# Performance work log

Hardware: AMD Instinct MI355X
Metric: run time of the kernel (lower is better)

Reference implementation:

```python
import jax, jax.numpy as jnp
import numpy as np

T, B, D, H, NQ = 512, 128, 512, 64, 64  # seq_len, batch, input_dim, hidden_dim == n_qubits
EPS = 1e-5

def setup_inputs() -> dict:
    key = jax.random.key(0)
    ks = jax.random.split(key, 11)
    s = 0.05
    return {
        "inputs": jax.random.normal(ks[0], (T, B, D), jnp.float32),
        "W0": jax.random.normal(ks[1], (4, NQ, D + H), jnp.float32) * s,
        "b0": jax.random.normal(ks[2], (4, NQ), jnp.float32) * s,
        "th0": jax.random.normal(ks[3], (4, NQ), jnp.float32) * s,
        "g0": jnp.ones((H,), jnp.float32),
        "be0": jnp.zeros((H,), jnp.float32),
        "W1": jax.random.normal(ks[4], (4, NQ, H + H), jnp.float32) * s,
        "b1": jax.random.normal(ks[5], (4, NQ), jnp.float32) * s,
        "th1": jax.random.normal(ks[6], (4, NQ), jnp.float32) * s,
        "g1": jnp.ones((H,), jnp.float32),
        "be1": jnp.zeros((H,), jnp.float32),
    }

def _qlstm_layer(x, W, b, th, gamma, beta):
    # x: [T, B, Din]. Faithful to source: h_prev = c_prev = 0 at EVERY timestep
    # (the torch code never writes back `states` inside the time loop), so all
    # timesteps are independent and fully vectorized.
    zeros_h = jnp.zeros(x.shape[:-1] + (H,), x.dtype)
    combined = jnp.concatenate([x, zeros_h], axis=-1)           # [T,B,Din+H]
    # 4 gate linears stacked on leading axis g: forget, input, update, output
    z = jnp.einsum('tbk,gnk->gtbn', combined, W) + b[:, None, None, :]
    # quantum circuit closed form: RX(z_i+th_i) per qubit + CNOT ladder + <Z_k>
    #   => cumprod_{i<=k} cos(z_i + th_i)
    q = jnp.cumprod(jnp.cos(z + th[:, None, None, :]), axis=-1)  # [4,T,B,NQ]
    sg = jax.nn.sigmoid(q)
    i_g = sg[1]
    g_g = jnp.tanh(sg[2])
    o_g = sg[3]
    # c = f * c_prev + i * g, with c_prev == 0  (f gate has no effect)
    c = i_g * g_g                                                # [T,B,H]
    h = o_g * jnp.tanh(c)
    mu = jnp.mean(h, axis=-1, keepdims=True)
    var = jnp.mean((h - mu) ** 2, axis=-1, keepdims=True)
    h_ln = (h - mu) * jax.lax.rsqrt(var + EPS) * gamma + beta
    return h_ln, c

def reference(inputs, W0, b0, th0, g0, be0, W1, b1, th1, g1, be1):
    h0, c0 = _qlstm_layer(inputs, W0, b0, th0, g0, be0)  # layer 0 (no dropout: p=0)
    h1, c1 = _qlstm_layer(h0, W1, b1, th1, g1, be1)      # layer 1
    outputs = h1                                          # [T,B,H]
    # new_states = states at the last timestep: [(h_ln, c)] per layer
    return (outputs, h0[-1], c0[-1], h1[-1], c1[-1])
```

## Files before the change

kernel.cpp:

```cpp
#include <hip/hip_runtime.h>
#include <hip/hip_bf16.h>

typedef __attribute__((ext_vector_type(8))) short bf16x8;
typedef __attribute__((ext_vector_type(4))) float f32x4;

#define T_SEQ   512
#define B_BATCH 128
#define H_DIM   64
#define MB      64
#define AS_STRIDE 136
#define ZS_STRIDE 193
#define A2S       72
#define LASTROW ((T_SEQ - 1) * B_BATCH)

#define W0H 0
#define W0M 98304
#define W0L 196608
#define W1H 294912
#define W1M 307200
#define W1L 319488

__device__ __forceinline__ void tsplit(float f, unsigned& h, unsigned& m, unsigned& l) {
    unsigned uf = __builtin_bit_cast(unsigned, f);
    h = uf >> 16;
    float hf = __builtin_bit_cast(float, uf & 0xFFFF0000u);
    float r1 = f - hf;
    unsigned u1 = __builtin_bit_cast(unsigned, r1);
    m = u1 >> 16;
    float mf = __builtin_bit_cast(float, u1 & 0xFFFF0000u);
    float r2 = r1 - mf;
    l = __builtin_bit_cast(unsigned, r2) >> 16;
}

__device__ __forceinline__ void tsplit2(float a, float b,
                                        unsigned& ph, unsigned& pm, unsigned& pl) {
    unsigned ha, ma, la, hb, mb, lb;
    tsplit(a, ha, ma, la);
    tsplit(b, hb, mb, lb);
    ph = ha | (hb << 16);
    pm = ma | (mb << 16);
    pl = la | (lb << 16);
}

__device__ __forceinline__ f32x4 mfma6(bf16x8 ah, bf16x8 am, bf16x8 al,
                                       bf16x8 bh, bf16x8 bm, bf16x8 bl, f32x4 c) {
    c = __builtin_amdgcn_mfma_f32_16x16x32_bf16(ah, bh, c, 0, 0, 0);
    c = __builtin_amdgcn_mfma_f32_16x16x32_bf16(ah, bm, c, 0, 0, 0);
    c = __builtin_amdgcn_mfma_f32_16x16x32_bf16(am, bh, c, 0, 0, 0);
    c = __builtin_amdgcn_mfma_f32_16x16x32_bf16(ah, bl, c, 0, 0, 0);
    c = __builtin_amdgcn_mfma_f32_16x16x32_bf16(al, bh, c, 0, 0, 0);
    c = __builtin_amdgcn_mfma_f32_16x16x32_bf16(am, bm, c, 0, 0, 0);
    return c;
}

__device__ __forceinline__ float fast_cos(float x) {
    float n = rintf(x * 0.6366197723675814f);
    int   m = (int)n;
    float r = __builtin_fmaf(n, -1.5707962512969971e+00f, x);
    r = __builtin_fmaf(n, -7.5497894158615964e-08f, r);
    r = __builtin_fmaf(n, -5.3903025299577647e-15f, r);
    float r2 = r * r;
    float ps = __builtin_fmaf(r2, 2.7557314297e-06f, -1.9841270114e-04f);
    ps = __builtin_fmaf(r2, ps, 8.3333337680e-03f);
    ps = __builtin_fmaf(r2, ps, -1.6666667163e-01f);
    float s = __builtin_fmaf(r * r2, ps, r);
    float pc = __builtin_fmaf(r2, 2.4801587642e-05f, -1.3888889225e-03f);
    pc = __builtin_fmaf(r2, pc, 4.1666667908e-02f);
    pc = __builtin_fmaf(r2, pc, -0.5f);
    float c = __builtin_fmaf(r2, pc, 1.0f);
    float v = (m & 1) ? s : c;
    unsigned sign = (unsigned)((m + 1) & 2) << 30;
    return __builtin_bit_cast(float, __builtin_bit_cast(unsigned, v) ^ sign);
}

__device__ __forceinline__ float fast_sigmoid(float x) {
    float e = __expf(-x);
    float d = 1.0f + e;
    float r = __builtin_amdgcn_rcpf(d);
    return r * (2.0f - d * r);
}

__device__ __forceinline__ float fast_tanh_pos(float x) {
    float t = __expf(2.0f * x);
    float d = t + 1.0f;
    float r = __builtin_amdgcn_rcpf(d);
    r = r * (2.0f - d * r);
    return (t - 1.0f) * r;
}

__global__ __launch_bounds__(256) void presplit_w(const float* __restrict__ W0,
                                                  const float* __restrict__ W1,
                                                  short* __restrict__ ws) {
    int i = blockIdx.x * 256 + threadIdx.x;
    if (i < 98304) {
        int r = i >> 9, k = i & 511;
        unsigned h, m, l;
        tsplit(W0[(r + 64) * 576 + k], h, m, l);
        ws[W0H + i] = (short)h;
        ws[W0M + i] = (short)m;
        ws[W0L + i] = (short)l;
    } else if (i < 110592) {
        int j = i - 98304;
        int r = j >> 6, k = j & 63;
        unsigned h, m, l;
        tsplit(W1[(r + 64) * 128 + k], h, m, l);
        ws[W1H + j] = (short)h;
        ws[W1M + j] = (short)m;
        ws[W1L + j] = (short)l;
    }
}

__global__ __launch_bounds__(256, 3) void qlstm_fused(
    const float* __restrict__ x,
    const float* __restrict__ b0,
    const float* __restrict__ th0,
    const float* __restrict__ g0,
    const float* __restrict__ be0,
    const float* __restrict__ b1,
    const float* __restrict__ th1,
    const float* __restrict__ g1,
    const float* __restrict__ be1,
    const short* __restrict__ wsp,
    float* __restrict__ out)
{
    __shared__ __align__(16) char lds[53760];
    short* ah = (short*)lds;
    short* am = ah + 64 * AS_STRIDE;
    short* al = am + 64 * AS_STRIDE;
    float* zs  = (float*)lds;
    short* a2h = (short*)lds;
    short* a2m = a2h + 64 * A2S;
    short* a2l = a2m + 64 * A2S;
    float* bt0 = (float*)(lds + 52224);
    float* bt1 = bt0 + 192;

    const int tid = threadIdx.x;
    const long rowbase = (long)blockIdx.x * MB;

    float* out0 = out;
    float* out1 = out + (long)T_SEQ * B_BATCH * H_DIM;
    float* out2 = out1 + B_BATCH * H_DIM;
    float* out3 = out2 + B_BATCH * H_DIM;
    float* out4 = out3 + B_BATCH * H_DIM;

    if (tid < 192) {
        bt0[tid] = b0[64 + tid] + th0[64 + tid];
        bt1[tid] = b1[64 + tid] + th1[64 + tid];
    }

    const int lane = tid & 63;
    const int wave = tid >> 6;
    const int ln   = lane & 15;
    const int quad = lane >> 4;
    const int cw   = wave * 48;

    int brow0[3], brow1[3];
    for (int nt = 0; nt < 3; ++nt) {
        int gc = cw + nt * 16 + ln;
        brow0[nt] = gc * 512;
        brow1[nt] = gc * 64;
    }

    f32x4 acc[4][3];
    for (int mt = 0; mt < 4; ++mt)
        for (int nt = 0; nt < 3; ++nt)
            acc[mt][nt] = (f32x4){0.f, 0.f, 0.f, 0.f};

    for (int kc = 0; kc < 512; kc += 128) {
        for (int pass = 0; pass < 4; ++pass) {
            int e  = pass * 256 + tid;
            int r  = e >> 4;
            int k8 = (e & 15) << 3;
            const float* xp = x + (rowbase + r) * 512 + kc + k8;
            float4 f0 = *(const float4*)xp;
            float4 f1 = *(const float4*)(xp + 4);
            uint4 Ph, Pm, Pl;
            tsplit2(f0.x, f0.y, Ph.x, Pm.x, Pl.x);
            tsplit2(f0.z, f0.w, Ph.y, Pm.y, Pl.y);
            tsplit2(f1.x, f1.y, Ph.z, Pm.z, Pl.z);
            tsplit2(f1.z, f1.w, Ph.w, Pm.w, Pl.w);
            int ao = r * AS_STRIDE + k8;
            *(uint4*)(ah + ao) = Ph;
            *(uint4*)(am + ao) = Pm;
            *(uint4*)(al + ao) = Pl;
        }
        __syncthreads();
        for (int k0 = 0; k0 < 128; k0 += 32) {
            int ka = k0 + quad * 8;
            bf16x8 Ah[4], Am[4], Al[4];
            for (int mt = 0; mt < 4; ++mt) {
                int ao = (mt * 16 + ln) * AS_STRIDE + ka;
                Ah[mt] = *(const bf16x8*)(ah + ao);
                Am[mt] = *(const bf16x8*)(am + ao);
                Al[mt] = *(const bf16x8*)(al + ao);
            }
            for (int nt = 0; nt < 3; ++nt) {
                int bo = brow0[nt] + kc + ka;
                bf16x8 Bh = *(const bf16x8*)(wsp + W0H + bo);
                bf16x8 Bm = *(const bf16x8*)(wsp + W0M + bo);
                bf16x8 Bl = *(const bf16x8*)(wsp + W0L + bo);
                for (int mt = 0; mt < 4; ++mt)
                    acc[mt][nt] = mfma6(Ah[mt], Am[mt], Al[mt], Bh, Bm, Bl, acc[mt][nt]);
            }
        }
        __syncthreads();
    }

    for (int mt = 0; mt < 4; ++mt)
        for (int nt = 0; nt < 3; ++nt)
            for (int i = 0; i < 4; ++i) {
                int row = mt * 16 + quad * 4 + i;
                int col = cw + nt * 16 + ln;
                zs[row * ZS_STRIDE + col] = acc[mt][nt][i];
            }
    __syncthreads();

    if (tid < 192) {
        int gi = tid >> 6;
        int r  = tid & 63;
        float* zrow = zs + r * ZS_STRIDE + gi * 64;
        const float* btg = bt0 + gi * 64;
        float p = 1.0f;
        for (int n = 0; n < 64; ++n) {
            p *= fast_cos(zrow[n] + btg[n]);
            zrow[n] = p;
        }
    }
    __syncthreads();

    {
        int r = tid >> 2;
        int j = tid & 3;
        long tbrow = rowbase + r;
        bool lastt = (tbrow >= LASTROW);
        int bidx = (int)(tbrow - LASTROW);
        const float* zr = zs + r * ZS_STRIDE;
        float h[16];
        float s = 0.f;
        for (int i = 0; i < 16; ++i) {
            int n = j * 16 + i;
            float q1 = zr[n];
            float q2 = zr[64 + n];
            float q3 = zr[128 + n];
            float ig = fast_sigmoid(q1);
            float gg = fast_tanh_pos(fast_sigmoid(q2));
            float og = fast_sigmoid(q3);
            float c  = ig * gg;
            float hv = og * fast_tanh_pos(c);
            h[i] = hv;
            s += hv;
            if (lastt) out2[bidx * 64 + n] = c;
        }
        s += __shfl_xor(s, 1);  s += __shfl_xor(s, 2);
        float mu = s * (1.0f / 64.0f);
        float s2 = 0.f;
        for (int i = 0; i < 16; ++i) {
            float d = h[i] - mu;
            s2 += d * d;
        }
        s2 += __shfl_xor(s2, 1); s2 += __shfl_xor(s2, 2);
        float var = s2 * (1.0f / 64.0f);
        float rs  = rsqrtf(var + 1e-5f);
        float hl[16];
        for (int i = 0; i < 16; ++i) {
            int n = j * 16 + i;
            hl[i] = (h[i] - mu) * rs * g0[n] + be0[n];
            if (lastt) out1[bidx * 64 + n] = hl[i];
        }
        __syncthreads();

        int ab = r * A2S + j * 16;
        uint4 Ph, Pm, Pl;
        tsplit2(hl[0], hl[1], Ph.x, Pm.x, Pl.x);
        tsplit2(hl[2], hl[3], Ph.y, Pm.y, Pl.y);
        tsplit2(hl[4], hl[5], Ph.z, Pm.z, Pl.z);
        tsplit2(hl[6], hl[7], Ph.w, Pm.w, Pl.w);
        *(uint4*)(a2h + ab) = Ph;
        *(uint4*)(a2m + ab) = Pm;
        *(uint4*)(a2l + ab) = Pl;
        tsplit2(hl[8],  hl[9],  Ph.x, Pm.x, Pl.x);
        tsplit2(hl[10], hl[11], Ph.y, Pm.y, Pl.y);
        tsplit2(hl[12], hl[13], Ph.z, Pm.z, Pl.z);
        tsplit2(hl[14], hl[15], Ph.w, Pm.w, Pl.w);
        *(uint4*)(a2h + ab + 8) = Ph;
        *(uint4*)(a2m + ab + 8) = Pm;
        *(uint4*)(a2l + ab + 8) = Pl;
    }
    __syncthreads();

    f32x4 acc2[4][3];
    for (int mt = 0; mt < 4; ++mt)
        for (int nt = 0; nt < 3; ++nt)
            acc2[mt][nt] = (f32x4){0.f, 0.f, 0.f, 0.f};
    for (int k0 = 0; k0 < 64; k0 += 32) {
        int ka = k0 + quad * 8;
        bf16x8 Ah[4], Am[4], Al[4];
        for (int mt = 0; mt < 4; ++mt) {
            int ao = (mt * 16 + ln) * A2S + ka;
            Ah[mt] = *(const bf16x8*)(a2h + ao);
            Am[mt] = *(const bf16x8*)(a2m + ao);
            Al[mt] = *(const bf16x8*)(a2l + ao);
        }
        for (int nt = 0; nt < 3; ++nt) {
            int bo = brow1[nt] + ka;
            bf16x8 Bh = *(const bf16x8*)(wsp + W1H + bo);
            bf16x8 Bm = *(const bf16x8*)(wsp + W1M + bo);
            bf16x8 Bl = *(const bf16x8*)(wsp + W1L + bo);
            for (int mt = 0; mt < 4; ++mt)
                acc2[mt][nt] = mfma6(Ah[mt], Am[mt], Al[mt], Bh, Bm, Bl, acc2[mt][nt]);
        }
    }
    __syncthreads();
    for (int mt = 0; mt < 4; ++mt)
        for (int nt = 0; nt < 3; ++nt)
            for (int i = 0; i < 4; ++i) {
                int row = mt * 16 + quad * 4 + i;
                int col = cw + nt * 16 + ln;
                zs[row * ZS_STRIDE + col] = acc2[mt][nt][i];
            }
    __syncthreads();

    if (tid < 192) {
        int gi = tid >> 6;
        int r  = tid & 63;
        float* zrow = zs + r * ZS_STRIDE + gi * 64;
        const float* btg = bt1 + gi * 64;
        float p = 1.0f;
        for (int n = 0; n < 64; ++n) {
            p *= fast_cos(zrow[n] + btg[n]);
            zrow[n] = p;
        }
    }
    __syncthreads();

    {
        int r = tid >> 2;
        int j = tid & 3;
        long tbrow = rowbase + r;
        bool lastt = (tbrow >= LASTROW);
        int bidx = (int)(tbrow - LASTROW);
        const float* zr = zs + r * ZS_STRIDE;
        float h[16];
        float s = 0.f;
        for (int i = 0; i < 16; ++i) {
            int n = j * 16 + i;
            float q1 = zr[n];
            float q2 = zr[64 + n];
            float q3 = zr[128 + n];
            float ig = fast_sigmoid(q1);
            float gg = fast_tanh_pos(fast_sigmoid(q2));
            float og = fast_sigmoid(q3);
            float c  = ig * gg;
            float hv = og * fast_tanh_pos(c);
            h[i] = hv;
            s += hv;
            if (lastt) out4[bidx * 64 + n] = c;
        }
        s += __shfl_xor(s, 1);  s += __shfl_xor(s, 2);
        float mu = s * (1.0f / 64.0f);
        float s2 = 0.f;
        for (int i = 0; i < 16; ++i) {
            float d = h[i] - mu;
            s2 += d * d;
        }
        s2 += __shfl_xor(s2, 1); s2 += __shfl_xor(s2, 2);
        float var = s2 * (1.0f / 64.0f);
        float rs  = rsqrtf(var + 1e-5f);
        float o4[16];
        for (int i = 0; i < 16; ++i)
            o4[i] = (h[i] - mu) * rs * g1[j * 16 + i] + be1[j * 16 + i];
        float* dst = out0 + tbrow * 64 + j * 16;
        for (int i4 = 0; i4 < 4; ++i4)
            *(float4*)(dst + i4 * 4) = *(float4*)(o4 + i4 * 4);
        if (lastt) {
            float* dst3 = out3 + (long)bidx * 64 + j * 16;
            for (int i4 = 0; i4 < 4; ++i4)
                *(float4*)(dst3 + i4 * 4) = *(float4*)(o4 + i4 * 4);
        }
    }
}

extern "C" void kernel_launch(void* const* d_in, const int* in_sizes, int n_in,
                              void* d_out, int out_size, void* d_ws, size_t ws_size,
                              hipStream_t stream) {
    const float* x   = (const float*)d_in[0];
    const float* W0  = (const float*)d_in[1];
    const float* b0  = (const float*)d_in[2];
    const float* th0 = (const float*)d_in[3];
    const float* g0  = (const float*)d_in[4];
    const float* be0 = (const float*)d_in[5];
    const float* W1  = (const float*)d_in[6];
    const float* b1  = (const float*)d_in[7];
    const float* th1 = (const float*)d_in[8];
    const float* g1  = (const float*)d_in[9];
    const float* be1 = (const float*)d_in[10];
    short* wsp = (short*)d_ws;

    presplit_w<<<dim3(432), dim3(256), 0, stream>>>(W0, W1, wsp);
    qlstm_fused<<<dim3(1024), dim3(256), 0, stream>>>(
        x, b0, th0, g0, be0, b1, th1, g1, be1, wsp, (float*)d_out);
}
```

Baseline: 323.2 us.

## Prefetch next input K-chunk into registers during MFMA on current chunk

The layer-0 GEMM now stages input in 64-wide K chunks instead of 128. Each thread loads the next chunk's 16 floats into registers before running the MFMAs on the current chunk, then splits and stores them to LDS after a barrier. This hides global-load latency behind compute and shrinks LDS usage, which may help occupancy. The cost is twice as many barriers, extra registers for the prefetch, and full unroll pragmas that can raise register pressure.

```diff
diff --git a/kernel.cpp b/kernel.cpp
--- a/kernel.cpp
+++ b/kernel.cpp
@@ -8,7 +8,7 @@
 #define B_BATCH 128
 #define H_DIM   64
 #define MB      64
-#define AS_STRIDE 136
+#define A1S     72
 #define ZS_STRIDE 193
 #define A2S       72
 #define LASTROW ((T_SEQ - 1) * B_BATCH)
@@ -40,6 +40,26 @@
     ph = ha | (hb << 16);
     pm = ma | (mb << 16);
     pl = la | (lb << 16);
+}
+
+__device__ __forceinline__ void split16(const float4 f[4],
+                                        short* __restrict__ ah, short* __restrict__ am,
+                                        short* __restrict__ al, int ao) {
+    uint4 Ph, Pm, Pl;
+    tsplit2(f[0].x, f[0].y, Ph.x, Pm.x, Pl.x);
+    tsplit2(f[0].z, f[0].w, Ph.y, Pm.y, Pl.y);
+    tsplit2(f[1].x, f[1].y, Ph.z, Pm.z, Pl.z);
+    tsplit2(f[1].z, f[1].w, Ph.w, Pm.w, Pl.w);
+    *(uint4*)(ah + ao) = Ph;
+    *(uint4*)(am + ao) = Pm;
+    *(uint4*)(al + ao) = Pl;
+    tsplit2(f[2].x, f[2].y, Ph.x, Pm.x, Pl.x);
+    tsplit2(f[2].z, f[2].w, Ph.y, Pm.y, Pl.y);
+    tsplit2(f[3].x, f[3].y, Ph.z, Pm.z, Pl.z);
+    tsplit2(f[3].z, f[3].w, Ph.w, Pm.w, Pl.w);
+    *(uint4*)(ah + ao + 8) = Ph;
+    *(uint4*)(am + ao + 8) = Pm;
+    *(uint4*)(al + ao + 8) = Pl;
 }
 
 __device__ __forceinline__ f32x4 mfma6(bf16x8 ah, bf16x8 am, bf16x8 al,
@@ -123,15 +143,15 @@
     const short* __restrict__ wsp,
     float* __restrict__ out)
 {
-    __shared__ __align__(16) char lds[53760];
+    __shared__ __align__(16) char lds[50944];
     short* ah = (short*)lds;
-    short* am = ah + 64 * AS_STRIDE;
-    short* al = am + 64 * AS_STRIDE;
+    short* am = ah + 64 * A1S;
+    short* al = am + 64 * A1S;
     float* zs  = (float*)lds;
     short* a2h = (short*)lds;
     short* a2m = a2h + 64 * A2S;
     short* a2l = a2m + 64 * A2S;
-    float* bt0 = (float*)(lds + 52224);
+    float* bt0 = (float*)(lds + 49408);
     float* bt1 = bt0 + 192;
 
     const int tid = threadIdx.x;
@@ -161,53 +181,68 @@
         brow1[nt] = gc * 64;
     }
 
+    const int sr = tid >> 2;
+    const int sc = (tid & 3) << 4;
+    const float* xrow = x + (rowbase + sr) * 512 + sc;
+    const int sao = sr * A1S + sc;
+
     f32x4 acc[4][3];
+    #pragma unroll
     for (int mt = 0; mt < 4; ++mt)
+        #pragma unroll
         for (int nt = 0; nt < 3; ++nt)
             acc[mt][nt] = (f32x4){0.f, 0.f, 0.f, 0.f};
 
-    for (int kc = 0; kc < 512; kc += 128) {
-        for (int pass = 0; pass < 4; ++pass) {
-            int e  = pass * 256 + tid;
-            int r  = e >> 4;
-            int k8 = (e & 15) << 3;
-            const float* xp = x + (rowbase + r) * 512 + kc + k8;
-            float4 f0 = *(const float4*)xp;
-            float4 f1 = *(const float4*)(xp + 4);
-            uint4 Ph, Pm, Pl;
-            tsplit2(f0.x, f0.y, Ph.x, Pm.x, Pl.x);
-            tsplit2(f0.z, f0.w, Ph.y, Pm.y, Pl.y);
-            tsplit2(f1.x, f1.y, Ph.z, Pm.z, Pl.z);
-            tsplit2(f1.z, f1.w, Ph.w, Pm.w, Pl.w);
-            int ao = r * AS_STRIDE + k8;
-            *(uint4*)(ah + ao) = Ph;
-            *(uint4*)(am + ao) = Pm;
-            *(uint4*)(al + ao) = Pl;
-        }
-        __syncthreads();
-        for (int k0 = 0; k0 < 128; k0 += 32) {
+    {
+        float4 f[4];
+        #pragma unroll
+        for (int u = 0; u < 4; ++u) f[u] = *(const float4*)(xrow + u * 4);
+        split16(f, ah, am, al, sao);
+    }
+    __syncthreads();
+
+    for (int kc = 0; kc < 512; kc += 64) {
+        float4 nf[4];
+        const bool more = (kc + 64) < 512;
+        if (more) {
+            #pragma unroll
+            for (int u = 0; u < 4; ++u)
+                nf[u] = *(const float4*)(xrow + kc + 64 + u * 4);
+        }
+        #pragma unroll
+        for (int k0 = 0; k0 < 64; k0 += 32) {
             int ka = k0 + quad * 8;
             bf16x8 Ah[4], Am[4], Al[4];
+            #pragma unroll
             for (int mt = 0; mt < 4; ++mt) {
-                int ao = (mt * 16 + ln) * AS_STRIDE + ka;
+                int ao = (mt * 16 + ln) * A1S + ka;
                 Ah[mt] = *(const bf16x8*)(ah + ao);
                 Am[mt] = *(const bf16x8*)(am + ao);
                 Al[mt] = *(const bf16x8*)(al + ao);
             }
+            #pragma unroll
             for (int nt = 0; nt < 3; ++nt) {
                 int bo = brow0[nt] + kc + ka;
                 bf16x8 Bh = *(const bf16x8*)(wsp + W0H + bo);
                 bf16x8 Bm = *(const bf16x8*)(wsp + W0M + bo);
                 bf16x8 Bl = *(const bf16x8*)(wsp + W0L + bo);
+                #pragma unroll
                 for (int mt = 0; mt < 4; ++mt)
                     acc[mt][nt] = mfma6(Ah[mt], Am[mt], Al[mt], Bh, Bm, Bl, acc[mt][nt]);
             }
         }
         __syncthreads();
-    }
-
+        if (more) {
+            split16(nf, ah, am, al, sao);
+            __syncthreads();
+        }
+    }
+
+    #pragma unroll
     for (int mt = 0; mt < 4; ++mt)
+        #pragma unroll
         for (int nt = 0; nt < 3; ++nt)
+            #pragma unroll
             for (int i = 0; i < 4; ++i) {
                 int row = mt * 16 + quad * 4 + i;
                 int col = cw + nt * 16 + ln;
@@ -237,6 +272,7 @@
         const float* zr = zs + r * ZS_STRIDE;
         float h[16];
         float s = 0.f;
+        #pragma unroll
         for (int i = 0; i < 16; ++i) {
             int n = j * 16 + i;
             float q1 = zr[n];
@@ -254,6 +290,7 @@
         s += __shfl_xor(s, 1);  s += __shfl_xor(s, 2);
         float mu = s * (1.0f / 64.0f);
         float s2 = 0.f;
+        #pragma unroll
         for (int i = 0; i < 16; ++i) {
             float d = h[i] - mu;
             s2 += d * d;
@@ -262,6 +299,7 @@
         float var = s2 * (1.0f / 64.0f);
         float rs  = rsqrtf(var + 1e-5f);
         float hl[16];
+        #pragma unroll
         for (int i = 0; i < 16; ++i) {
             int n = j * 16 + i;
             hl[i] = (h[i] - mu) * rs * g0[n] + be0[n];
@@ -289,30 +327,39 @@
     __syncthreads();
 
     f32x4 acc2[4][3];
+    #pragma unroll
     for (int mt = 0; mt < 4; ++mt)
+        #pragma unroll
         for (int nt = 0; nt < 3; ++nt)
             acc2[mt][nt] = (f32x4){0.f, 0.f, 0.f, 0.f};
+    #pragma unroll
     for (int k0 = 0; k0 < 64; k0 += 32) {
         int ka = k0 + quad * 8;
         bf16x8 Ah[4], Am[4], Al[4];
+        #pragma unroll
         for (int mt = 0; mt < 4; ++mt) {
             int ao = (mt * 16 + ln) * A2S + ka;
             Ah[mt] = *(const bf16x8*)(a2h + ao);
             Am[mt] = *(const bf16x8*)(a2m + ao);
             Al[mt] = *(const bf16x8*)(a2l + ao);
         }
+        #pragma unroll
         for (int nt = 0; nt < 3; ++nt) {
             int bo = brow1[nt] + ka;
             bf16x8 Bh = *(const bf16x8*)(wsp + W1H + bo);
             bf16x8 Bm = *(const bf16x8*)(wsp + W1M + bo);
             bf16x8 Bl = *(const bf16x8*)(wsp + W1L + bo);
+            #pragma unroll
             for (int mt = 0; mt < 4; ++mt)
                 acc2[mt][nt] = mfma6(Ah[mt], Am[mt], Al[mt], Bh, Bm, Bl, acc2[mt][nt]);
         }
     }
     __syncthreads();
+    #pragma unroll
     for (int mt = 0; mt < 4; ++mt)
+        #pragma unroll
         for (int nt = 0; nt < 3; ++nt)
+            #pragma unroll
             for (int i = 0; i < 4; ++i) {
                 int row = mt * 16 + quad * 4 + i;
                 int col = cw + nt * 16 + ln;
@@ -342,6 +389,7 @@
         const float* zr = zs + r * ZS_STRIDE;
         float h[16];
         float s = 0.f;
+        #pragma unroll
         for (int i = 0; i < 16; ++i) {
             int n = j * 16 + i;
             float q1 = zr[n];
@@ -359,6 +407,7 @@
         s += __shfl_xor(s, 1);  s += __shfl_xor(s, 2);
         float mu = s * (1.0f / 64.0f);
         float s2 = 0.f;
+        #pragma unroll
         for (int i = 0; i < 16; ++i) {
             float d = h[i] - mu;
             s2 += d * d;
@@ -367,13 +416,16 @@
         float var = s2 * (1.0f / 64.0f);
         float rs  = rsqrtf(var + 1e-5f);
         float o4[16];
+        #pragma unroll
         for (int i = 0; i < 16; ++i)
             o4[i] = (h[i] - mu) * rs * g1[j * 16 + i] + be1[j * 16 + i];
         float* dst = out0 + tbrow * 64 + j * 16;
+        #pragma unroll
         for (int i4 = 0; i4 < 4; ++i4)
             *(float4*)(dst + i4 * 4) = *(float4*)(o4 + i4 * 4);
         if (lastt) {
             float* dst3 = out3 + (long)bidx * 64 + j * 16;
+            #pragma unroll
             for (int i4 = 0; i4 < 4; ++i4)
                 *(float4*)(dst3 + i4 * 4) = *(float4*)(o4 + i4 * 4);
         }
```

Result: no change. 321.9 us (-0.4%).
